# Kernel tuning notes

Hardware: AMD Instinct MI355X
Metric: run time of the kernel (lower is better)

Reference implementation:

```python
import jax, jax.numpy as jnp
import numpy as np

E = 256   # hidden_dim
H = 2     # num_heads
DH = E // H
EPS = 1e-5


def setup_inputs() -> dict:
    key = jax.random.key(0)
    ks = jax.random.split(key, 20)
    L, S, MAXLOOP = 8192, 8192, 16
    rel = jax.random.randint(ks[0], (L, MAXLOOP), 0, S)
    # sprinkle some padding sentinels (-1 / -2) like real edge loops
    pad = jax.random.uniform(ks[1], (L, MAXLOOP)) < 0.25
    rel = jnp.where(pad, -1, rel)
    rel = rel.at[:, 0].set(jnp.abs(rel[:, 0]) % S)  # ensure >=1 valid edge per face
    inp = {
        'v_face_edge_loop': rel.astype(jnp.int64) if jax.config.jax_enable_x64 else rel.astype(jnp.int32),
        'v_face_mask': jnp.ones((L,), dtype=bool),
        'v_edge_embedding': jax.random.normal(ks[2], (S, E), jnp.float32),
        'v_face_embedding': jax.random.normal(ks[3], (L, E), jnp.float32),
    }
    def w(k, shape):
        return (jax.random.normal(k, shape, jnp.float32) * 0.02)
    for i, base in ((1, 4), (2, 10)):
        inp[f'w_in{i}'] = w(ks[base + 0], (3 * E, E))
        inp[f'b_in{i}'] = jnp.zeros((3 * E,), jnp.float32)
        inp[f'w_out{i}'] = w(ks[base + 1], (E, E))
        inp[f'b_out{i}'] = jnp.zeros((E,), jnp.float32)
        inp[f'ln{i}_g'] = jnp.ones((E,), jnp.float32)
        inp[f'ln{i}_b'] = jnp.zeros((E,), jnp.float32)
    return inp


def _build_mask(face_edge_loop, S):
    # True = disallowed (torch bool attn_mask semantics).
    L = face_edge_loop.shape[0]
    rel = face_edge_loop
    invalid = (rel == -1) | (rel == -2)
    rel = jnp.where(invalid, S, rel)  # scatter invalids into sentinel column S
    mask = jnp.ones((L, S + 1), dtype=bool)
    mask = mask.at[jnp.arange(L)[:, None], rel].set(False)
    return mask[:, :S]  # [L, S]


def _mha(x, kv, mask, w_in, b_in, w_out, b_out):
    # torch nn.MultiheadAttention (unbatched, eval/no-dropout)
    wq, wk, wv = jnp.split(w_in, 3, axis=0)
    bq, bk, bv = jnp.split(b_in, 3, axis=0)
    L, S = x.shape[0], kv.shape[0]
    q = (x @ wq.T + bq).reshape(L, H, DH)
    k = (kv @ wk.T + bk).reshape(S, H, DH)
    v = (kv @ wv.T + bv).reshape(S, H, DH)
    scores = jnp.einsum('lhd,shd->hls', q, k) / np.sqrt(DH).astype(np.float32)
    scores = jnp.where(mask[None, :, :], jnp.float32(-1e9), scores)
    attn = jax.nn.softmax(scores, axis=-1)          # [H, L, S]
    out = jnp.einsum('hls,shd->lhd', attn, v).reshape(L, E)
    return out @ w_out.T + b_out


def _layernorm(x, g, b):
    m = x.mean(-1, keepdims=True)
    var = ((x - m) ** 2).mean(-1, keepdims=True)
    return (x - m) / jnp.sqrt(var + EPS) * g + b


def reference(v_face_edge_loop, v_face_mask, v_edge_embedding, v_face_embedding,
              w_in1, b_in1, w_out1, b_out1, ln1_g, ln1_b,
              w_in2, b_in2, w_out2, b_out2, ln2_g, ln2_b):
    S = v_edge_embedding.shape[0]
    # v_face_mask is all-True here (static shapes); loop[mask] == loop
    mask = _build_mask(v_face_edge_loop, S)
    x = v_face_embedding
    x = x + _mha(x, v_edge_embedding, mask, w_in1, b_in1, w_out1, b_out1)
    x = _layernorm(x, ln1_g, ln1_b)
    x = x + _mha(x, v_edge_embedding, mask, w_in2, b_in2, w_out2, b_out2)
    x = _layernorm(x, ln2_g, ln2_b)
    return x
```

## Files before the change

kernel.cpp:

```cpp
#include <hip/hip_runtime.h>
#include <hip/hip_bf16.h>

typedef short short8 __attribute__((ext_vector_type(8)));
typedef short short4v __attribute__((ext_vector_type(4)));
typedef float f32x4 __attribute__((ext_vector_type(4)));

#define E 256
#define DH 128

__device__ __forceinline__ float bf2f(__hip_bfloat16 x) { return __bfloat162float(x); }
__device__ __forceinline__ __hip_bfloat16 f2bf(float x) { return __float2bfloat16(x); }

struct CvtArgs { const float* in[6]; __hip_bfloat16* out[6]; int n[6]; };

__global__ __launch_bounds__(256) void f2b_all(CvtArgs a)
{
    int seg = blockIdx.y;
    int i = (blockIdx.x * 256 + threadIdx.x) * 8;
    if (i >= a.n[seg]) return;
    const float* in = a.in[seg];
    float4 x = *reinterpret_cast<const float4*>(in + i);
    float4 y = *reinterpret_cast<const float4*>(in + i + 4);
    __hip_bfloat16* o = a.out[seg] + i;
    o[0] = f2bf(x.x); o[1] = f2bf(x.y); o[2] = f2bf(x.z); o[3] = f2bf(x.w);
    o[4] = f2bf(y.x); o[5] = f2bf(y.y); o[6] = f2bf(y.z); o[7] = f2bf(y.w);
}

struct ProjSeg { const __hip_bfloat16* A; const __hip_bfloat16* W; const float* b; __hip_bfloat16* out; };
struct ProjArgs { ProjSeg seg[5]; };

__global__ __launch_bounds__(256) void gemm_proj(ProjArgs args, int M)
{
    int wv = threadIdx.x >> 6, lane = threadIdx.x & 63;
    int m0 = blockIdx.x * 32;
    if (m0 >= M) return;
    ProjSeg sg = args.seg[blockIdx.y];
    int lo = lane & 15, hi = lane >> 4;

    const __hip_bfloat16* arow0 = sg.A + (size_t)(m0 + lo) * E + hi * 8;
    const __hip_bfloat16* arow1 = arow0 + 16 * E;
    const __hip_bfloat16* brow  = sg.W + (size_t)(wv * 64 + lo) * E + hi * 8;

    f32x4 acc[2][4] = {};
#pragma unroll
    for (int k = 0; k < 8; ++k) {
        short8 a0 = *reinterpret_cast<const short8*>(arow0 + k * 32);
        short8 a1 = *reinterpret_cast<const short8*>(arow1 + k * 32);
#pragma unroll
        for (int nt = 0; nt < 4; ++nt) {
            short8 b = *reinterpret_cast<const short8*>(brow + (size_t)nt * 16 * E + k * 32);
            acc[0][nt] = __builtin_amdgcn_mfma_f32_16x16x32_bf16(a0, b, acc[0][nt], 0, 0, 0);
            acc[1][nt] = __builtin_amdgcn_mfma_f32_16x16x32_bf16(a1, b, acc[1][nt], 0, 0, 0);
        }
    }
#pragma unroll
    for (int nt = 0; nt < 4; ++nt) {
        int col = wv * 64 + nt * 16 + lo;
        float bias = sg.b[col];
#pragma unroll
        for (int mt = 0; mt < 2; ++mt)
#pragma unroll
            for (int r = 0; r < 4; ++r) {
                int row = m0 + mt * 16 + hi * 4 + r;
                sg.out[(size_t)row * E + col] = f2bf(acc[mt][nt][r] + bias);
            }
    }
}

__global__ __launch_bounds__(1024) void attn_outproj_ln(
    const int* __restrict__ rel, const __hip_bfloat16* __restrict__ q16,
    const __hip_bfloat16* __restrict__ k16, const __hip_bfloat16* __restrict__ v16,
    const __hip_bfloat16* __restrict__ wout, const float* __restrict__ bout,
    const float* __restrict__ resid, const float* __restrict__ lng, const float* __restrict__ lnb,
    const __hip_bfloat16* __restrict__ wq_next, const float* __restrict__ bq_next,
    float* __restrict__ xres_out, __hip_bfloat16* __restrict__ qnext_out,
    float* __restrict__ final_out, int L, int ML)
{
    __shared__ __align__(16) __hip_bfloat16 atile[16 * 264];
    __shared__ __align__(16) float sm[16 * 260];
    __shared__ __align__(16) float lds_w[16][2][16];
    __shared__ int lds_idx[16][16];

    int tid = threadIdx.x, wv = tid >> 6, lane = tid & 63;
    int m0 = blockIdx.x * 16;
    int g = lane >> 2, q = lane & 3;
    int face = m0 + wv;
    const float scale = 0.088388347648318447f;

    const int* rr = rel + (size_t)face * ML;
    int myidx = (g < ML) ? rr[g] : -1;

    bool dup = false;
#pragma unroll
    for (int d = 1; d < 16; ++d) {
        int other = __shfl(myidx, ((g - d) & 15) * 4 + q);
        if (d <= g && other == myidx) dup = true;
    }
    bool myuse = (myidx >= 0) && !dup;
    int safe = myidx < 0 ? 0 : myidx;
    if (q == 0) lds_idx[wv][g] = safe;

#pragma unroll
    for (int h = 0; h < 2; ++h) {
        const __hip_bfloat16* kbase = k16 + (size_t)safe * E + h * DH;
        const __hip_bfloat16* qbase = q16 + (size_t)face * E + h * DH;
        float part = 0.f;
#pragma unroll
        for (int t = 0; t < 4; ++t) {
            short8 qv = *reinterpret_cast<const short8*>(qbase + (t * 4 + q) * 8);
            short8 kv = *reinterpret_cast<const short8*>(kbase + (t * 4 + q) * 8);
            const __hip_bfloat16* qp = (const __hip_bfloat16*)&qv;
            const __hip_bfloat16* kp = (const __hip_bfloat16*)&kv;
#pragma unroll
            for (int e2 = 0; e2 < 8; ++e2)
                part += bf2f(qp[e2]) * bf2f(kp[e2]);
        }
        part += __shfl_xor(part, 1);
        part += __shfl_xor(part, 2);
        float sc = myuse ? part * scale : -1e30f;
        float mx = sc;
#pragma unroll
        for (int off = 4; off < 64; off <<= 1) mx = fmaxf(mx, __shfl_xor(mx, off));
        float e = __expf(sc - mx);
        float den = e;
#pragma unroll
        for (int off = 4; off < 64; off <<= 1) den += __shfl_xor(den, off);
        if (q == 0) lds_w[wv][h][g] = e / den;
    }

    {
        int h = lane >> 5;
        float a0 = 0.f, a1 = 0.f, a2 = 0.f, a3 = 0.f;
#pragma unroll
        for (int j = 0; j < 16; ++j) {
            int ij = lds_idx[wv][j];
            float wj = lds_w[wv][h][j];
            short4v vv = *reinterpret_cast<const short4v*>(v16 + (size_t)ij * E + 4 * lane);
            const __hip_bfloat16* vp = (const __hip_bfloat16*)&vv;
            a0 += wj * bf2f(vp[0]);
            a1 += wj * bf2f(vp[1]);
            a2 += wj * bf2f(vp[2]);
            a3 += wj * bf2f(vp[3]);
        }
        __hip_bfloat16 ob[4] = {f2bf(a0), f2bf(a1), f2bf(a2), f2bf(a3)};
        *reinterpret_cast<short4v*>(atile + wv * 264 + 4 * lane) =
            *reinterpret_cast<const short4v*>(ob);
    }
    __syncthreads();

    {
        int lo = lane & 15, hi = lane >> 4;
        const __hip_bfloat16* arow = atile + lo * 264 + hi * 8;
        const __hip_bfloat16* brow = wout + (size_t)(wv * 16 + lo) * E + hi * 8;
        f32x4 acc = {0.f, 0.f, 0.f, 0.f};
#pragma unroll
        for (int kk = 0; kk < 8; ++kk) {
            short8 a = *reinterpret_cast<const short8*>(arow + kk * 32);
            short8 b = *reinterpret_cast<const short8*>(brow + kk * 32);
            acc = __builtin_amdgcn_mfma_f32_16x16x32_bf16(a, b, acc, 0, 0, 0);
        }
        int col = wv * 16 + lo;
#pragma unroll
        for (int r = 0; r < 4; ++r)
            sm[(hi * 4 + r) * 260 + col] = acc[r];
    }
    __syncthreads();

    {
        int rowg = m0 + wv;
        float4 pv = *reinterpret_cast<const float4*>(sm + wv * 260 + 4 * lane);
        float4 rv = *reinterpret_cast<const float4*>(resid + (size_t)rowg * E + 4 * lane);
        float4 bb = *reinterpret_cast<const float4*>(bout + 4 * lane);
        float v0 = pv.x + bb.x + rv.x;
        float v1 = pv.y + bb.y + rv.y;
        float v2 = pv.z + bb.z + rv.z;
        float v3 = pv.w + bb.w + rv.w;
        float s  = v0 + v1 + v2 + v3;
        float s2 = v0 * v0 + v1 * v1 + v2 * v2 + v3 * v3;
#pragma unroll
        for (int off = 1; off < 64; off <<= 1) {
            s  += __shfl_xor(s, off);
            s2 += __shfl_xor(s2, off);
        }
        float mean = s * (1.f / 256.f);
        float var  = s2 * (1.f / 256.f) - mean * mean;
        float rstd = rsqrtf(var + 1e-5f);
        float4 gg = *reinterpret_cast<const float4*>(lng + 4 * lane);
        float4 b2 = *reinterpret_cast<const float4*>(lnb + 4 * lane);
        float y0 = (v0 - mean) * rstd * gg.x + b2.x;
        float y1 = (v1 - mean) * rstd * gg.y + b2.y;
        float y2 = (v2 - mean) * rstd * gg.z + b2.z;
        float y3 = (v3 - mean) * rstd * gg.w + b2.w;
        if (final_out) {
            float4 o = {y0, y1, y2, y3};
            *reinterpret_cast<float4*>(final_out + (size_t)rowg * E + 4 * lane) = o;
        } else {
            float4 o = {y0, y1, y2, y3};
            *reinterpret_cast<float4*>(xres_out + (size_t)rowg * E + 4 * lane) = o;
            __hip_bfloat16 ob[4] = {f2bf(y0), f2bf(y1), f2bf(y2), f2bf(y3)};
            *reinterpret_cast<short4v*>(atile + wv * 264 + 4 * lane) =
                *reinterpret_cast<const short4v*>(ob);
        }
    }

    if (qnext_out) {
        __syncthreads();
        int lo = lane & 15, hi = lane >> 4;
        const __hip_bfloat16* arow = atile + lo * 264 + hi * 8;
        const __hip_bfloat16* brow = wq_next + (size_t)(wv * 16 + lo) * E + hi * 8;
        f32x4 acc = {0.f, 0.f, 0.f, 0.f};
#pragma unroll
        for (int kk = 0; kk < 8; ++kk) {
            short8 a = *reinterpret_cast<const short8*>(arow + kk * 32);
            short8 b = *reinterpret_cast<const short8*>(brow + kk * 32);
            acc = __builtin_amdgcn_mfma_f32_16x16x32_bf16(a, b, acc, 0, 0, 0);
        }
        int col = wv * 16 + lo;
        float bias = bq_next[col];
#pragma unroll
        for (int r = 0; r < 4; ++r)
            qnext_out[(size_t)(m0 + hi * 4 + r) * E + col] = f2bf(acc[r] + bias);
    }
}

extern "C" void kernel_launch(void* const* d_in, const int* in_sizes, int n_in,
                              void* d_out, int out_size, void* d_ws, size_t ws_size,
                              hipStream_t stream) {
    const int* rel = (const int*)d_in[0];
    const float* edge = (const float*)d_in[2];
    const float* face = (const float*)d_in[3];
    const float* w_in[2]  = {(const float*)d_in[4],  (const float*)d_in[10]};
    const float* b_in[2]  = {(const float*)d_in[5],  (const float*)d_in[11]};
    const float* w_out[2] = {(const float*)d_in[6],  (const float*)d_in[12]};
    const float* b_out[2] = {(const float*)d_in[7],  (const float*)d_in[13]};
    const float* ln_g[2]  = {(const float*)d_in[8],  (const float*)d_in[14]};
    const float* ln_b[2]  = {(const float*)d_in[9],  (const float*)d_in[15]};

    int S = in_sizes[2] / E;
    int L = in_sizes[3] / E;
    int ML = in_sizes[0] / L;

    char* ws = (char*)d_ws;
    __hip_bfloat16* face16 = (__hip_bfloat16*)ws; ws += (size_t)L * E * 2;
    __hip_bfloat16* edge16 = (__hip_bfloat16*)ws; ws += (size_t)S * E * 2;
    __hip_bfloat16* q16    = (__hip_bfloat16*)ws; ws += (size_t)L * E * 2;
    __hip_bfloat16* k16[2], *v16[2];
    for (int l = 0; l < 2; ++l) {
        k16[l] = (__hip_bfloat16*)ws; ws += (size_t)S * E * 2;
        v16[l] = (__hip_bfloat16*)ws; ws += (size_t)S * E * 2;
    }
    float* xres = (float*)ws;                     ws += (size_t)L * E * 4;
    __hip_bfloat16* win16[2], *wout16[2];
    for (int l = 0; l < 2; ++l) {
        win16[l]  = (__hip_bfloat16*)ws; ws += (size_t)3 * E * E * 2;
        wout16[l] = (__hip_bfloat16*)ws; ws += (size_t)E * E * 2;
    }

    float* outp = (float*)d_out;

    {
        CvtArgs ca;
        ca.in[0] = face;     ca.out[0] = face16;    ca.n[0] = L * E;
        ca.in[1] = edge;     ca.out[1] = edge16;    ca.n[1] = S * E;
        ca.in[2] = w_in[0];  ca.out[2] = win16[0];  ca.n[2] = 3 * E * E;
        ca.in[3] = w_in[1];  ca.out[3] = win16[1];  ca.n[3] = 3 * E * E;
        ca.in[4] = w_out[0]; ca.out[4] = wout16[0]; ca.n[4] = E * E;
        ca.in[5] = w_out[1]; ca.out[5] = wout16[1]; ca.n[5] = E * E;
        int gx = (L * E) / (256 * 8);
        f2b_all<<<dim3(gx, 6), 256, 0, stream>>>(ca);
    }

    {
        ProjArgs pa;
        pa.seg[0] = {face16, win16[0],                     b_in[0],         q16};
        pa.seg[1] = {edge16, win16[0] + (size_t)E * E,     b_in[0] + E,     k16[0]};
        pa.seg[2] = {edge16, win16[0] + (size_t)2 * E * E, b_in[0] + 2 * E, v16[0]};
        pa.seg[3] = {edge16, win16[1] + (size_t)E * E,     b_in[1] + E,     k16[1]};
        pa.seg[4] = {edge16, win16[1] + (size_t)2 * E * E, b_in[1] + 2 * E, v16[1]};
        gemm_proj<<<dim3(L / 32, 5), 256, 0, stream>>>(pa, L);
    }

    attn_outproj_ln<<<L / 16, 1024, 0, stream>>>(rel, q16, k16[0], v16[0],
                                                 wout16[0], b_out[0], face,
                                                 ln_g[0], ln_b[0],
                                                 win16[1], b_in[1],
                                                 xres, q16, nullptr, L, ML);

    attn_outproj_ln<<<L / 16, 1024, 0, stream>>>(rel, q16, k16[1], v16[1],
                                                 wout16[1], b_out[1], xres,
                                                 ln_g[1], ln_b[1],
                                                 nullptr, nullptr,
                                                 nullptr, nullptr, outp, L, ML);
}
```

Measured before the change: 179.4 us.

## Fuse fp32-to-bf16 conversion into projection GEMM and drop separate convert kernel

Measured after the change: 198.7 us. 10.7% more time.

```diff
diff --git a/kernel.cpp b/kernel.cpp
--- a/kernel.cpp
+++ b/kernel.cpp
@@ -11,58 +11,71 @@
 __device__ __forceinline__ float bf2f(__hip_bfloat16 x) { return __bfloat162float(x); }
 __device__ __forceinline__ __hip_bfloat16 f2bf(float x) { return __float2bfloat16(x); }
 
-struct CvtArgs { const float* in[6]; __hip_bfloat16* out[6]; int n[6]; };
-
-__global__ __launch_bounds__(256) void f2b_all(CvtArgs a)
+__device__ __forceinline__ short8 ld8cvt(const float* p) {
+    float4 x = *reinterpret_cast<const float4*>(p);
+    float4 y = *reinterpret_cast<const float4*>(p + 4);
+    __hip_bfloat16 h[8] = {f2bf(x.x), f2bf(x.y), f2bf(x.z), f2bf(x.w),
+                           f2bf(y.x), f2bf(y.y), f2bf(y.z), f2bf(y.w)};
+    return *reinterpret_cast<const short8*>(h);
+}
+
+struct ProjArgs2 {
+    const float* A[5]; const float* W[5]; const float* b[5]; __hip_bfloat16* out[5];
+    const float* cvin[3]; __hip_bfloat16* cvout[3];
+};
+
+__global__ __launch_bounds__(256) void gemm_proj_cvt(ProjArgs2 args, int M)
 {
-    int seg = blockIdx.y;
-    int i = (blockIdx.x * 256 + threadIdx.x) * 8;
-    if (i >= a.n[seg]) return;
-    const float* in = a.in[seg];
-    float4 x = *reinterpret_cast<const float4*>(in + i);
-    float4 y = *reinterpret_cast<const float4*>(in + i + 4);
-    __hip_bfloat16* o = a.out[seg] + i;
-    o[0] = f2bf(x.x); o[1] = f2bf(x.y); o[2] = f2bf(x.z); o[3] = f2bf(x.w);
-    o[4] = f2bf(y.x); o[5] = f2bf(y.y); o[6] = f2bf(y.z); o[7] = f2bf(y.w);
-}
-
-struct ProjSeg { const __hip_bfloat16* A; const __hip_bfloat16* W; const float* b; __hip_bfloat16* out; };
-struct ProjArgs { ProjSeg seg[5]; };
-
-__global__ __launch_bounds__(256) void gemm_proj(ProjArgs args, int M)
-{
+    if (blockIdx.y == 5) {
+        int bx = blockIdx.x;
+        if (bx >= 96) return;
+        const float* in = args.cvin[bx >> 5];
+        __hip_bfloat16* out = args.cvout[bx >> 5];
+        int i = ((bx & 31) * 256 + threadIdx.x) * 8;
+        float4 x = *reinterpret_cast<const float4*>(in + i);
+        float4 y = *reinterpret_cast<const float4*>(in + i + 4);
+        __hip_bfloat16* o = out + i;
+        o[0] = f2bf(x.x); o[1] = f2bf(x.y); o[2] = f2bf(x.z); o[3] = f2bf(x.w);
+        o[4] = f2bf(y.x); o[5] = f2bf(y.y); o[6] = f2bf(y.z); o[7] = f2bf(y.w);
+        return;
+    }
+
     int wv = threadIdx.x >> 6, lane = threadIdx.x & 63;
     int m0 = blockIdx.x * 32;
     if (m0 >= M) return;
-    ProjSeg sg = args.seg[blockIdx.y];
+    int seg = blockIdx.y;
+    const float* A = args.A[seg];
+    const float* W = args.W[seg];
     int lo = lane & 15, hi = lane >> 4;
 
-    const __hip_bfloat16* arow0 = sg.A + (size_t)(m0 + lo) * E + hi * 8;
-    const __hip_bfloat16* arow1 = arow0 + 16 * E;
-    const __hip_bfloat16* brow  = sg.W + (size_t)(wv * 64 + lo) * E + hi * 8;
+    const float* arow0 = A + (size_t)(m0 + lo) * E + hi * 8;
+    const float* arow1 = arow0 + 16 * E;
+    const float* brow  = W + (size_t)(wv * 64 + lo) * E + hi * 8;
 
     f32x4 acc[2][4] = {};
 #pragma unroll
     for (int k = 0; k < 8; ++k) {
-        short8 a0 = *reinterpret_cast<const short8*>(arow0 + k * 32);
-        short8 a1 = *reinterpret_cast<const short8*>(arow1 + k * 32);
+        short8 a0 = ld8cvt(arow0 + k * 32);
+        short8 a1 = ld8cvt(arow1 + k * 32);
 #pragma unroll
         for (int nt = 0; nt < 4; ++nt) {
-            short8 b = *reinterpret_cast<const short8*>(brow + (size_t)nt * 16 * E + k * 32);
+            short8 b = ld8cvt(brow + (size_t)nt * 16 * E + k * 32);
             acc[0][nt] = __builtin_amdgcn_mfma_f32_16x16x32_bf16(a0, b, acc[0][nt], 0, 0, 0);
             acc[1][nt] = __builtin_amdgcn_mfma_f32_16x16x32_bf16(a1, b, acc[1][nt], 0, 0, 0);
         }
     }
+    const float* bias_p = args.b[seg];
+    __hip_bfloat16* out = args.out[seg];
 #pragma unroll
     for (int nt = 0; nt < 4; ++nt) {
         int col = wv * 64 + nt * 16 + lo;
-        float bias = sg.b[col];
+        float bias = bias_p[col];
 #pragma unroll
         for (int mt = 0; mt < 2; ++mt)
 #pragma unroll
             for (int r = 0; r < 4; ++r) {
                 int row = m0 + mt * 16 + hi * 4 + r;
-                sg.out[(size_t)row * E + col] = f2bf(acc[mt][nt][r] + bias);
+                out[(size_t)row * E + col] = f2bf(acc[mt][nt][r] + bias);
             }
     }
 }
@@ -104,17 +117,20 @@
     for (int h = 0; h < 2; ++h) {
         const __hip_bfloat16* kbase = k16 + (size_t)safe * E + h * DH;
         const __hip_bfloat16* qbase = q16 + (size_t)face * E + h * DH;
-        float part = 0.f;
+        float p0 = 0.f, p1 = 0.f, p2 = 0.f, p3 = 0.f;
 #pragma unroll
         for (int t = 0; t < 4; ++t) {
             short8 qv = *reinterpret_cast<const short8*>(qbase + (t * 4 + q) * 8);
             short8 kv = *reinterpret_cast<const short8*>(kbase + (t * 4 + q) * 8);
             const __hip_bfloat16* qp = (const __hip_bfloat16*)&qv;
             const __hip_bfloat16* kp = (const __hip_bfloat16*)&kv;
+            float s0 = 0.f;
 #pragma unroll
             for (int e2 = 0; e2 < 8; ++e2)
-                part += bf2f(qp[e2]) * bf2f(kp[e2]);
-        }
+                s0 += bf2f(qp[e2]) * bf2f(kp[e2]);
+            if (t == 0) p0 = s0; else if (t == 1) p1 = s0; else if (t == 2) p2 = s0; else p3 = s0;
+        }
+        float part = (p0 + p1) + (p2 + p3);
         part += __shfl_xor(part, 1);
         part += __shfl_xor(part, 2);
         float sc = myuse ? part * scale : -1e30f;
@@ -241,8 +257,6 @@
     int ML = in_sizes[0] / L;
 
     char* ws = (char*)d_ws;
-    __hip_bfloat16* face16 = (__hip_bfloat16*)ws; ws += (size_t)L * E * 2;
-    __hip_bfloat16* edge16 = (__hip_bfloat16*)ws; ws += (size_t)S * E * 2;
     __hip_bfloat16* q16    = (__hip_bfloat16*)ws; ws += (size_t)L * E * 2;
     __hip_bfloat16* k16[2], *v16[2];
     for (int l = 0; l < 2; ++l) {
@@ -250,40 +264,29 @@
         v16[l] = (__hip_bfloat16*)ws; ws += (size_t)S * E * 2;
     }
     float* xres = (float*)ws;                     ws += (size_t)L * E * 4;
-    __hip_bfloat16* win16[2], *wout16[2];
-    for (int l = 0; l < 2; ++l) {
-        win16[l]  = (__hip_bfloat16*)ws; ws += (size_t)3 * E * E * 2;
-        wout16[l] = (__hip_bfloat16*)ws; ws += (size_t)E * E * 2;
-    }
+    __hip_bfloat16* wout16[2];
+    for (int l = 0; l < 2; ++l) { wout16[l] = (__hip_bfloat16*)ws; ws += (size_t)E * E * 2; }
+    __hip_bfloat16* wq1_16 = (__hip_bfloat16*)ws; ws += (size_t)E * E * 2;
 
     float* outp = (float*)d_out;
 
     {
-        CvtArgs ca;
-        ca.in[0] = face;     ca.out[0] = face16;    ca.n[0] = L * E;
-        ca.in[1] = edge;     ca.out[1] = edge16;    ca.n[1] = S * E;
-        ca.in[2] = w_in[0];  ca.out[2] = win16[0];  ca.n[2] = 3 * E * E;
-        ca.in[3] = w_in[1];  ca.out[3] = win16[1];  ca.n[3] = 3 * E * E;
-        ca.in[4] = w_out[0]; ca.out[4] = wout16[0]; ca.n[4] = E * E;
-        ca.in[5] = w_out[1]; ca.out[5] = wout16[1]; ca.n[5] = E * E;
-        int gx = (L * E) / (256 * 8);
-        f2b_all<<<dim3(gx, 6), 256, 0, stream>>>(ca);
-    }
-
-    {
-        ProjArgs pa;
-        pa.seg[0] = {face16, win16[0],                     b_in[0],         q16};
-        pa.seg[1] = {edge16, win16[0] + (size_t)E * E,     b_in[0] + E,     k16[0]};
-        pa.seg[2] = {edge16, win16[0] + (size_t)2 * E * E, b_in[0] + 2 * E, v16[0]};
-        pa.seg[3] = {edge16, win16[1] + (size_t)E * E,     b_in[1] + E,     k16[1]};
-        pa.seg[4] = {edge16, win16[1] + (size_t)2 * E * E, b_in[1] + 2 * E, v16[1]};
-        gemm_proj<<<dim3(L / 32, 5), 256, 0, stream>>>(pa, L);
+        ProjArgs2 pa;
+        pa.A[0] = face; pa.W[0] = w_in[0];                     pa.b[0] = b_in[0];         pa.out[0] = q16;
+        pa.A[1] = edge; pa.W[1] = w_in[0] + (size_t)E * E;     pa.b[1] = b_in[0] + E;     pa.out[1] = k16[0];
+        pa.A[2] = edge; pa.W[2] = w_in[0] + (size_t)2 * E * E; pa.b[2] = b_in[0] + 2 * E; pa.out[2] = v16[0];
+        pa.A[3] = edge; pa.W[3] = w_in[1] + (size_t)E * E;     pa.b[3] = b_in[1] + E;     pa.out[3] = k16[1];
+        pa.A[4] = edge; pa.W[4] = w_in[1] + (size_t)2 * E * E; pa.b[4] = b_in[1] + 2 * E; pa.out[4] = v16[1];
+        pa.cvin[0] = w_out[0]; pa.cvout[0] = wout16[0];
+        pa.cvin[1] = w_out[1]; pa.cvout[1] = wout16[1];
+        pa.cvin[2] = w_in[1];  pa.cvout[2] = wq1_16;
+        gemm_proj_cvt<<<dim3(L / 32, 6), 256, 0, stream>>>(pa, L);
     }
 
     attn_outproj_ln<<<L / 16, 1024, 0, stream>>>(rel, q16, k16[0], v16[0],
                                                  wout16[0], b_out[0], face,
                                                  ln_g[0], ln_b[0],
-                                                 win16[1], b_in[1],
+                                                 wq1_16, b_in[1],
                                                  xres, q16, nullptr, L, ML);
 
     attn_outproj_ln<<<L / 16, 1024, 0, stream>>>(rel, q16, k16[1], v16[1],
```

## Stage projection GEMM tiles through swizzled LDS with double-buffered global_load_lds

Applied to the files above, without the earlier changes.

Result: faster. 167.9 us (median of 2 runs) (-6.4%).

```diff
diff --git a/kernel.cpp b/kernel.cpp
--- a/kernel.cpp
+++ b/kernel.cpp
@@ -29,30 +29,63 @@
 struct ProjSeg { const __hip_bfloat16* A; const __hip_bfloat16* W; const float* b; __hip_bfloat16* out; };
 struct ProjArgs { ProjSeg seg[5]; };
 
+#define GLDS(g, l) __builtin_amdgcn_global_load_lds( \
+    (const __attribute__((address_space(1))) void*)(g), \
+    (__attribute__((address_space(3))) void*)(l), 16, 0, 0)
+
 __global__ __launch_bounds__(256) void gemm_proj(ProjArgs args, int M)
 {
+    __shared__ __hip_bfloat16 sA[2][32 * 64];
+    __shared__ __hip_bfloat16 sW[2][256 * 64];
+
     int wv = threadIdx.x >> 6, lane = threadIdx.x & 63;
     int m0 = blockIdx.x * 32;
-    if (m0 >= M) return;
     ProjSeg sg = args.seg[blockIdx.y];
     int lo = lane & 15, hi = lane >> 4;
 
-    const __hip_bfloat16* arow0 = sg.A + (size_t)(m0 + lo) * E + hi * 8;
-    const __hip_bfloat16* arow1 = arow0 + 16 * E;
-    const __hip_bfloat16* brow  = sg.W + (size_t)(wv * 64 + lo) * E + hi * 8;
+    int lr = lane >> 3;
+    int lcol = ((lane & 7) ^ lr) * 8;
+
+    auto stage = [&](int buf, int kc) {
+        {
+            int R = wv * 8 + lr;
+            GLDS(sg.A + (size_t)(m0 + R) * E + kc * 64 + lcol, &sA[buf][(wv * 8) * 64]);
+        }
+#pragma unroll
+        for (int s = 0; s < 8; ++s) {
+            int R = wv * 64 + s * 8 + lr;
+            GLDS(sg.W + (size_t)R * E + kc * 64 + lcol, &sW[buf][(wv * 64 + s * 8) * 64]);
+        }
+    };
+
+    stage(0, 0);
+    __syncthreads();
 
     f32x4 acc[2][4] = {};
-#pragma unroll
-    for (int k = 0; k < 8; ++k) {
-        short8 a0 = *reinterpret_cast<const short8*>(arow0 + k * 32);
-        short8 a1 = *reinterpret_cast<const short8*>(arow1 + k * 32);
-#pragma unroll
-        for (int nt = 0; nt < 4; ++nt) {
-            short8 b = *reinterpret_cast<const short8*>(brow + (size_t)nt * 16 * E + k * 32);
-            acc[0][nt] = __builtin_amdgcn_mfma_f32_16x16x32_bf16(a0, b, acc[0][nt], 0, 0, 0);
-            acc[1][nt] = __builtin_amdgcn_mfma_f32_16x16x32_bf16(a1, b, acc[1][nt], 0, 0, 0);
-        }
-    }
+    const int swz = (lo & 7);
+#pragma unroll
+    for (int kc = 0; kc < 4; ++kc) {
+        int cur = kc & 1;
+        if (kc < 3) stage(cur ^ 1, kc + 1);
+
+        const char* aB = (const char*)sA[cur];
+        const char* wB = (const char*)sW[cur];
+#pragma unroll
+        for (int ks = 0; ks < 2; ++ks) {
+            int phys = ((hi + 4 * ks) ^ swz) * 16;
+            short8 a0 = *reinterpret_cast<const short8*>(aB + (0 * 16 + lo) * 128 + phys);
+            short8 a1 = *reinterpret_cast<const short8*>(aB + (1 * 16 + lo) * 128 + phys);
+#pragma unroll
+            for (int nt = 0; nt < 4; ++nt) {
+                short8 b = *reinterpret_cast<const short8*>(
+                    wB + (wv * 64 + nt * 16 + lo) * 128 + phys);
+                acc[0][nt] = __builtin_amdgcn_mfma_f32_16x16x32_bf16(a0, b, acc[0][nt], 0, 0, 0);
+                acc[1][nt] = __builtin_amdgcn_mfma_f32_16x16x32_bf16(a1, b, acc[1][nt], 0, 0, 0);
+            }
+        }
+        __syncthreads();
+    }
+
 #pragma unroll
     for (int nt = 0; nt < 4; ++nt) {
         int col = wv * 64 + nt * 16 + lo;
```
